# Optimization experiments

Measured on AMD Instinct MI355X. Metric: run time of the kernel, lower is better.

## Reference

```python
import jax, jax.numpy as jnp
import numpy as np

N = 65536   # num rois (batch*num_rois)
C = 512     # input_channels
D = 512     # output_dims = num_heads * head_dims
H = 8       # num_heads
HD = 64     # head_dims
L = 16      # hardcoded expand size in forward
BN_EPS = 1e-5


def _bn(x, gamma, beta, mean, var):
    # eval-mode BatchNorm1d over channel axis 1 of [N, D, L]
    inv = gamma / jnp.sqrt(var + BN_EPS)
    return x * inv[None, :, None] + (beta - mean * inv)[None, :, None]


def setup_inputs() -> dict:
    key = jax.random.key(0)
    ks = jax.random.split(key, 12)
    w = lambda k, shape: jax.random.normal(k, shape, jnp.float32) * 0.05
    return {
        "features": jax.random.normal(ks[0], (N, C), jnp.float32),
        "features2": jax.random.normal(ks[1], (N, C), jnp.float32),
        "Wk": w(ks[2], (D, C)),      # key_proj conv1d weight (shared for pos & key)
        "Wv1": w(ks[3], (D, C)),     # value_proj conv1d #1
        "Wv2": w(ks[4], (D, D)),     # value_proj conv1d #2
        "bn1_gamma": jnp.ones((D,), jnp.float32),
        "bn1_beta": jnp.zeros((D,), jnp.float32),
        "bn1_mean": jax.random.normal(ks[5], (D,), jnp.float32) * 0.1,
        "bn1_var": jax.random.uniform(ks[6], (D,), jnp.float32, 0.5, 1.5),
        "bn2_gamma": jnp.ones((D,), jnp.float32),
        "bn2_beta": jnp.zeros((D,), jnp.float32),
        "bn2_mean": jax.random.normal(ks[7], (D,), jnp.float32) * 0.1,
        "bn2_var": jax.random.uniform(ks[8], (D,), jnp.float32, 0.5, 1.5),
        "Wa": w(ks[9], (H, D)),      # attention_proj conv1d
        "Wqk": w(ks[10], (D, D)),    # qk_coef Linear
        "Wvc": w(ks[11], (D, D)),    # v_coef Linear
    }


def reference(features, features2, Wk, Wv1, Wv2,
              bn1_gamma, bn1_beta, bn1_mean, bn1_var,
              bn2_gamma, bn2_beta, bn2_mean, bn2_var,
              Wa, Wqk, Wvc):
    # expand [N, C] -> [N, C, L] (all L columns identical, as in torch .expand)
    f = jnp.broadcast_to(features[:, :, None], (features.shape[0], features.shape[1], L))
    f2 = jnp.broadcast_to(features2[:, :, None], (features2.shape[0], features2.shape[1], L))

    # key_proj (shared weights) on both inputs: 1x1 conv + ReLU
    pos = jax.nn.relu(jnp.einsum('oc,ncl->nol', Wk, f))
    key_e = jax.nn.relu(jnp.einsum('oc,ncl->nol', Wk, f2))

    # value_proj: conv -> BN -> ReLU -> conv -> BN -> ReLU
    h = jax.nn.relu(_bn(jnp.einsum('oc,ncl->nol', Wv1, f2), bn1_gamma, bn1_beta, bn1_mean, bn1_var))
    value = jax.nn.relu(_bn(jnp.einsum('od,ndl->nol', Wv2, h), bn2_gamma, bn2_beta, bn2_mean, bn2_var))

    pk = pos * key_e                                    # [N, D, L]
    v_coef = jax.nn.sigmoid(pos.mean(axis=2) @ Wvc.T)   # [N, D]
    qk_coef = jax.nn.sigmoid(pk.mean(axis=2) @ Wqk.T)   # [N, D]

    value = value + pos * v_coef[:, :, None]
    attn_emb = pk * qk_coef[:, :, None]

    attn = jnp.einsum('hd,ndl->nhl', Wa, attn_emb)      # [N, H, L]
    attn = jax.nn.softmax(attn, axis=-1)
    attn = jnp.repeat(attn, HD, axis=1)                 # [N, H*HD, L], head-major

    return jnp.sum(attn * value, axis=-1)               # [N, D]
```

## Files before the change

### kernel.cpp

```cpp
#include <hip/hip_runtime.h>
#include <hip/hip_bf16.h>
#include <cstdint>
#include <cstddef>


#define DIM 512
#define NROWS 65536
#define MBLK 64

typedef __bf16 bf16;
typedef __attribute__((ext_vector_type(8))) __bf16 bf16x8;
typedef __attribute__((ext_vector_type(4))) __bf16 bf16x4;
typedef __attribute__((ext_vector_type(4))) float f32x4;

__device__ __forceinline__ float sigmoidf_(float x) {
  return 1.0f / (1.0f + __expf(-x));
}

__device__ __forceinline__ int lds_off(int row, int cb) {
  return row * (DIM * 2) + (cb ^ ((row & 15) << 4));
}

__device__ __forceinline__ bf16x8 lda(const char* As, int i, int lr, int kq,
                                      int kb) {
  return *(const bf16x8*)(As + (i * 16 + lr) * (DIM * 2) +
                          ((kb * 2 + kq * 16) ^ (lr << 4)));
}

__global__ __launch_bounds__(256) void cvt4_f32_bf16(
    const float* __restrict__ s0, const float* __restrict__ s1,
    const float* __restrict__ s2, const float* __restrict__ s3,
    bf16* __restrict__ d0, bf16* __restrict__ d1, bf16* __restrict__ d2,
    bf16* __restrict__ d3) {
  int mat = blockIdx.x >> 8;
  int i = (blockIdx.x & 255) * 256 + threadIdx.x;
  const float* s = mat == 0 ? s0 : mat == 1 ? s1 : mat == 2 ? s2 : s3;
  bf16* d = mat == 0 ? d0 : mat == 1 ? d1 : mat == 2 ? d2 : d3;
  f32x4 v = ((const f32x4*)s)[i];
  bf16x4 o;
  o[0] = (bf16)v[0]; o[1] = (bf16)v[1]; o[2] = (bf16)v[2]; o[3] = (bf16)v[3];
  ((bf16x4*)d)[i] = o;
}

__device__ __forceinline__ void stage2(char* PA, const float* __restrict__ ga,
                                       char* PB, const float* __restrict__ gb,
                                       int t) {
#pragma unroll
  for (int it = 0; it < 4; ++it) {
    int c = it * 1024 + t;
    f32x4 a0 = *(const f32x4*)(ga + (size_t)c * 8);
    f32x4 a1 = *(const f32x4*)(ga + (size_t)c * 8 + 4);
    f32x4 b0 = *(const f32x4*)(gb + (size_t)c * 8);
    f32x4 b1 = *(const f32x4*)(gb + (size_t)c * 8 + 4);
    bf16x8 oa, ob;
    oa[0] = (bf16)a0[0]; oa[1] = (bf16)a0[1]; oa[2] = (bf16)a0[2]; oa[3] = (bf16)a0[3];
    oa[4] = (bf16)a1[0]; oa[5] = (bf16)a1[1]; oa[6] = (bf16)a1[2]; oa[7] = (bf16)a1[3];
    ob[0] = (bf16)b0[0]; ob[1] = (bf16)b0[1]; ob[2] = (bf16)b0[2]; ob[3] = (bf16)b0[3];
    ob[4] = (bf16)b1[0]; ob[5] = (bf16)b1[1]; ob[6] = (bf16)b1[2]; ob[7] = (bf16)b1[3];
    int off = lds_off(c >> 6, (c & 63) * 16);
    *(bf16x8*)(PA + off) = oa;
    *(bf16x8*)(PB + off) = ob;
  }
}

__device__ __forceinline__ void gemm_core(f32x4 (&acc)[4][2], const char* As,
                                          const bf16* __restrict__ W, int lr,
                                          int kq, int wn) {
  const bf16* bp = W + (size_t)(wn + lr) * DIM + kq * 8;
  bf16x8 a0[4], a1[4], b0[2], b1[2];
#pragma unroll
  for (int j = 0; j < 2; j++) b0[j] = *(const bf16x8*)(bp + j * 16 * DIM);
#pragma unroll
  for (int j = 0; j < 2; j++) b1[j] = *(const bf16x8*)(bp + j * 16 * DIM + 32);
#pragma unroll
  for (int i = 0; i < 4; i++) a0[i] = lda(As, i, lr, kq, 0);
#pragma unroll
  for (int kb = 0; kb < DIM; kb += 64) {
#pragma unroll
    for (int i = 0; i < 4; i++) a1[i] = lda(As, i, lr, kq, kb + 32);
#pragma unroll
    for (int i = 0; i < 4; i++)
#pragma unroll
      for (int j = 0; j < 2; j++)
        acc[i][j] = __builtin_amdgcn_mfma_f32_16x16x32_bf16(a0[i], b0[j],
                                                            acc[i][j], 0, 0, 0);
    if (kb + 64 < DIM) {
#pragma unroll
      for (int j = 0; j < 2; j++)
        b0[j] = *(const bf16x8*)(bp + j * 16 * DIM + kb + 64);
#pragma unroll
      for (int i = 0; i < 4; i++) a0[i] = lda(As, i, lr, kq, kb + 64);
    }
#pragma unroll
    for (int i = 0; i < 4; i++)
#pragma unroll
      for (int j = 0; j < 2; j++)
        acc[i][j] = __builtin_amdgcn_mfma_f32_16x16x32_bf16(a1[i], b1[j],
                                                            acc[i][j], 0, 0, 0);
    if (kb + 96 < DIM) {
#pragma unroll
      for (int j = 0; j < 2; j++)
        b1[j] = *(const bf16x8*)(bp + j * 16 * DIM + kb + 96);
    }
  }
}

__device__ __forceinline__ void zero_acc(f32x4 (&acc)[4][2]) {
#pragma unroll
  for (int i = 0; i < 4; i++)
#pragma unroll
    for (int j = 0; j < 2; j++) acc[i][j] = (f32x4){0.f, 0.f, 0.f, 0.f};
}

__global__ __launch_bounds__(1024, 1) void fused_all(
    const float* __restrict__ f, const float* __restrict__ f2,
    const bf16* __restrict__ Wk, const bf16* __restrict__ Wvc,
    const bf16* __restrict__ Wv1, const bf16* __restrict__ Wv2,
    float* __restrict__ out, const float* __restrict__ bg1,
    const float* __restrict__ bb1, const float* __restrict__ bm1,
    const float* __restrict__ bv1, const float* __restrict__ bg2,
    const float* __restrict__ bb2, const float* __restrict__ bm2,
    const float* __restrict__ bv2) {
  __shared__ __align__(16) char P1[MBLK * DIM * 2];
  __shared__ __align__(16) char P2[MBLK * DIM * 2];

  const int t = threadIdx.x;
  const int lane = t & 63;
  const int lr = lane & 15;
  const int kq = lane >> 4;
  const int wn = (t >> 6) * 32;
  const size_t m0 = (size_t)blockIdx.x * MBLK;

  stage2(P1, f + m0 * DIM, P2, f2 + m0 * DIM, t);
  __syncthreads();

  f32x4 acc[4][2];

  zero_acc(acc);
  gemm_core(acc, P1, Wk, lr, kq, wn);
  __syncthreads();
#pragma unroll
  for (int i = 0; i < 4; i++)
#pragma unroll
    for (int j = 0; j < 2; j++)
#pragma unroll
      for (int r = 0; r < 4; r++) {
        int m = i * 16 + kq * 4 + r;
        int n = wn + j * 16 + lr;
        *(bf16*)(P1 + lds_off(m, n * 2)) = (bf16)fmaxf(acc[i][j][r], 0.f);
      }
  __syncthreads();

  zero_acc(acc);
  gemm_core(acc, P1, Wvc, lr, kq, wn);
  bf16x4 pvr[4][2];
#pragma unroll
  for (int i = 0; i < 4; i++)
#pragma unroll
    for (int j = 0; j < 2; j++)
#pragma unroll
      for (int r = 0; r < 4; r++) {
        int m = i * 16 + kq * 4 + r;
        int n = wn + j * 16 + lr;
        float p = (float)(*(const bf16*)(P1 + lds_off(m, n * 2)));
        pvr[i][j][r] = (bf16)(sigmoidf_(acc[i][j][r]) * p);
      }

  zero_acc(acc);
  gemm_core(acc, P2, Wv1, lr, kq, wn);
  float iv1[2], bc1[2];
#pragma unroll
  for (int j = 0; j < 2; j++) {
    int c = wn + j * 16 + lr;
    float s = bg1[c] * rsqrtf(bv1[c] + 1e-5f);
    iv1[j] = s;
    bc1[j] = bb1[c] - bm1[c] * s;
  }
  __syncthreads();
#pragma unroll
  for (int i = 0; i < 4; i++)
#pragma unroll
    for (int j = 0; j < 2; j++)
#pragma unroll
      for (int r = 0; r < 4; r++) {
        int m = i * 16 + kq * 4 + r;
        int n = wn + j * 16 + lr;
        float v = fmaxf(acc[i][j][r] * iv1[j] + bc1[j], 0.f);
        *(bf16*)(P2 + lds_off(m, n * 2)) = (bf16)v;
      }
  __syncthreads();

  zero_acc(acc);
  gemm_core(acc, P2, Wv2, lr, kq, wn);
  float iv2[2], bc2[2];
#pragma unroll
  for (int j = 0; j < 2; j++) {
    int c = wn + j * 16 + lr;
    float s = bg2[c] * rsqrtf(bv2[c] + 1e-5f);
    iv2[j] = s;
    bc2[j] = bb2[c] - bm2[c] * s;
  }
#pragma unroll
  for (int i = 0; i < 4; i++)
#pragma unroll
    for (int j = 0; j < 2; j++)
#pragma unroll
      for (int r = 0; r < 4; r++) {
        int m = i * 16 + kq * 4 + r;
        int n = wn + j * 16 + lr;
        float v = fmaxf(acc[i][j][r] * iv2[j] + bc2[j], 0.f) + (float)pvr[i][j][r];
        out[(m0 + m) * DIM + n] = v;
      }
}

extern "C" void kernel_launch(void* const* d_in, const int* in_sizes, int n_in,
                              void* d_out, int out_size, void* d_ws,
                              size_t ws_size, hipStream_t stream) {
  const float* features  = (const float*)d_in[0];
  const float* features2 = (const float*)d_in[1];
  const float* Wk  = (const float*)d_in[2];
  const float* Wv1 = (const float*)d_in[3];
  const float* Wv2 = (const float*)d_in[4];
  const float* g1 = (const float*)d_in[5];
  const float* b1 = (const float*)d_in[6];
  const float* m1 = (const float*)d_in[7];
  const float* v1 = (const float*)d_in[8];
  const float* g2 = (const float*)d_in[9];
  const float* b2 = (const float*)d_in[10];
  const float* m2 = (const float*)d_in[11];
  const float* v2 = (const float*)d_in[12];
  const float* Wvc = (const float*)d_in[15];
  float* out = (float*)d_out;

  bf16* wkb  = (bf16*)d_ws;
  bf16* wvcb = wkb + (size_t)DIM * DIM;
  bf16* wv1b = wvcb + (size_t)DIM * DIM;
  bf16* wv2b = wv1b + (size_t)DIM * DIM;

  cvt4_f32_bf16<<<dim3(4 * 256), dim3(256), 0, stream>>>(
      Wk, Wvc, Wv1, Wv2, wkb, wvcb, wv1b, wv2b);

  dim3 grid(NROWS / MBLK);
  dim3 block(1024);
  fused_all<<<grid, block, 0, stream>>>(features, features2, wkb, wvcb, wv1b,
                                        wv2b, out, g1, b1, m1, v1, g2, b2, m2,
                                        v2);
}
```

Measured before the change: 664.5 us.

## Split fused kernel into two kernels with pv intermediate in workspace

Splits the single fused kernel into two. The first computes the pos and v_coef path and writes the gated pos*v_coef product to a bf16 workspace. The second computes the value path and adds the stored product. This halves LDS per block from 128KB to 64KB and removes the live pvr registers across GEMMs, which could allow two blocks per CU despite launch_bounds(1024,1). The cost is an extra round trip of a 64MB intermediate through global memory and a second launch.

```diff
diff --git a/kernel.cpp b/kernel.cpp
--- a/kernel.cpp
+++ b/kernel.cpp
@@ -42,24 +42,17 @@
   ((bf16x4*)d)[i] = o;
 }
 
-__device__ __forceinline__ void stage2(char* PA, const float* __restrict__ ga,
-                                       char* PB, const float* __restrict__ gb,
-                                       int t) {
+__device__ __forceinline__ void stage_panel(char* P, const float* __restrict__ g,
+                                            int t) {
 #pragma unroll
   for (int it = 0; it < 4; ++it) {
     int c = it * 1024 + t;
-    f32x4 a0 = *(const f32x4*)(ga + (size_t)c * 8);
-    f32x4 a1 = *(const f32x4*)(ga + (size_t)c * 8 + 4);
-    f32x4 b0 = *(const f32x4*)(gb + (size_t)c * 8);
-    f32x4 b1 = *(const f32x4*)(gb + (size_t)c * 8 + 4);
-    bf16x8 oa, ob;
-    oa[0] = (bf16)a0[0]; oa[1] = (bf16)a0[1]; oa[2] = (bf16)a0[2]; oa[3] = (bf16)a0[3];
-    oa[4] = (bf16)a1[0]; oa[5] = (bf16)a1[1]; oa[6] = (bf16)a1[2]; oa[7] = (bf16)a1[3];
-    ob[0] = (bf16)b0[0]; ob[1] = (bf16)b0[1]; ob[2] = (bf16)b0[2]; ob[3] = (bf16)b0[3];
-    ob[4] = (bf16)b1[0]; ob[5] = (bf16)b1[1]; ob[6] = (bf16)b1[2]; ob[7] = (bf16)b1[3];
-    int off = lds_off(c >> 6, (c & 63) * 16);
-    *(bf16x8*)(PA + off) = oa;
-    *(bf16x8*)(PB + off) = ob;
+    f32x4 v0 = *(const f32x4*)(g + (size_t)c * 8);
+    f32x4 v1 = *(const f32x4*)(g + (size_t)c * 8 + 4);
+    bf16x8 o;
+    o[0] = (bf16)v0[0]; o[1] = (bf16)v0[1]; o[2] = (bf16)v0[2]; o[3] = (bf16)v0[3];
+    o[4] = (bf16)v1[0]; o[5] = (bf16)v1[1]; o[6] = (bf16)v1[2]; o[7] = (bf16)v1[3];
+    *(bf16x8*)(P + lds_off(c >> 6, (c & 63) * 16)) = o;
   }
 }
 
@@ -112,17 +105,10 @@
     for (int j = 0; j < 2; j++) acc[i][j] = (f32x4){0.f, 0.f, 0.f, 0.f};
 }
 
-__global__ __launch_bounds__(1024, 1) void fused_all(
-    const float* __restrict__ f, const float* __restrict__ f2,
-    const bf16* __restrict__ Wk, const bf16* __restrict__ Wvc,
-    const bf16* __restrict__ Wv1, const bf16* __restrict__ Wv2,
-    float* __restrict__ out, const float* __restrict__ bg1,
-    const float* __restrict__ bb1, const float* __restrict__ bm1,
-    const float* __restrict__ bv1, const float* __restrict__ bg2,
-    const float* __restrict__ bb2, const float* __restrict__ bm2,
-    const float* __restrict__ bv2) {
-  __shared__ __align__(16) char P1[MBLK * DIM * 2];
-  __shared__ __align__(16) char P2[MBLK * DIM * 2];
+__global__ __launch_bounds__(1024, 1) void fusedA(
+    const float* __restrict__ f, const bf16* __restrict__ Wk,
+    const bf16* __restrict__ Wvc, bf16x4* __restrict__ pvws) {
+  __shared__ __align__(16) char P[MBLK * DIM * 2];
 
   const int t = threadIdx.x;
   const int lane = t & 63;
@@ -131,13 +117,13 @@
   const int wn = (t >> 6) * 32;
   const size_t m0 = (size_t)blockIdx.x * MBLK;
 
-  stage2(P1, f + m0 * DIM, P2, f2 + m0 * DIM, t);
+  stage_panel(P, f + m0 * DIM, t);
   __syncthreads();
 
   f32x4 acc[4][2];
 
   zero_acc(acc);
-  gemm_core(acc, P1, Wk, lr, kq, wn);
+  gemm_core(acc, P, Wk, lr, kq, wn);
   __syncthreads();
 #pragma unroll
   for (int i = 0; i < 4; i++)
@@ -147,27 +133,52 @@
       for (int r = 0; r < 4; r++) {
         int m = i * 16 + kq * 4 + r;
         int n = wn + j * 16 + lr;
-        *(bf16*)(P1 + lds_off(m, n * 2)) = (bf16)fmaxf(acc[i][j][r], 0.f);
-      }
-  __syncthreads();
-
-  zero_acc(acc);
-  gemm_core(acc, P1, Wvc, lr, kq, wn);
-  bf16x4 pvr[4][2];
-#pragma unroll
-  for (int i = 0; i < 4; i++)
-#pragma unroll
-    for (int j = 0; j < 2; j++)
-#pragma unroll
-      for (int r = 0; r < 4; r++) {
-        int m = i * 16 + kq * 4 + r;
-        int n = wn + j * 16 + lr;
-        float p = (float)(*(const bf16*)(P1 + lds_off(m, n * 2)));
-        pvr[i][j][r] = (bf16)(sigmoidf_(acc[i][j][r]) * p);
-      }
-
-  zero_acc(acc);
-  gemm_core(acc, P2, Wv1, lr, kq, wn);
+        *(bf16*)(P + lds_off(m, n * 2)) = (bf16)fmaxf(acc[i][j][r], 0.f);
+      }
+  __syncthreads();
+
+  zero_acc(acc);
+  gemm_core(acc, P, Wvc, lr, kq, wn);
+#pragma unroll
+  for (int i = 0; i < 4; i++)
+#pragma unroll
+    for (int j = 0; j < 2; j++) {
+      bf16x4 o;
+#pragma unroll
+      for (int r = 0; r < 4; r++) {
+        int m = i * 16 + kq * 4 + r;
+        int n = wn + j * 16 + lr;
+        float p = (float)(*(const bf16*)(P + lds_off(m, n * 2)));
+        o[r] = (bf16)(sigmoidf_(acc[i][j][r]) * p);
+      }
+      pvws[((size_t)blockIdx.x * 8 + i * 2 + j) * 1024 + t] = o;
+    }
+}
+
+__global__ __launch_bounds__(1024, 1) void fusedB(
+    const float* __restrict__ f2, const bf16* __restrict__ Wv1,
+    const bf16* __restrict__ Wv2, const bf16x4* __restrict__ pvws,
+    float* __restrict__ out, const float* __restrict__ bg1,
+    const float* __restrict__ bb1, const float* __restrict__ bm1,
+    const float* __restrict__ bv1, const float* __restrict__ bg2,
+    const float* __restrict__ bb2, const float* __restrict__ bm2,
+    const float* __restrict__ bv2) {
+  __shared__ __align__(16) char P[MBLK * DIM * 2];
+
+  const int t = threadIdx.x;
+  const int lane = t & 63;
+  const int lr = lane & 15;
+  const int kq = lane >> 4;
+  const int wn = (t >> 6) * 32;
+  const size_t m0 = (size_t)blockIdx.x * MBLK;
+
+  stage_panel(P, f2 + m0 * DIM, t);
+  __syncthreads();
+
+  f32x4 acc[4][2];
+
+  zero_acc(acc);
+  gemm_core(acc, P, Wv1, lr, kq, wn);
   float iv1[2], bc1[2];
 #pragma unroll
   for (int j = 0; j < 2; j++) {
@@ -186,12 +197,12 @@
         int m = i * 16 + kq * 4 + r;
         int n = wn + j * 16 + lr;
         float v = fmaxf(acc[i][j][r] * iv1[j] + bc1[j], 0.f);
-        *(bf16*)(P2 + lds_off(m, n * 2)) = (bf16)v;
-      }
-  __syncthreads();
-
-  zero_acc(acc);
-  gemm_core(acc, P2, Wv2, lr, kq, wn);
+        *(bf16*)(P + lds_off(m, n * 2)) = (bf16)v;
+      }
+  __syncthreads();
+
+  zero_acc(acc);
+  gemm_core(acc, P, Wv2, lr, kq, wn);
   float iv2[2], bc2[2];
 #pragma unroll
   for (int j = 0; j < 2; j++) {
@@ -203,14 +214,16 @@
 #pragma unroll
   for (int i = 0; i < 4; i++)
 #pragma unroll
-    for (int j = 0; j < 2; j++)
-#pragma unroll
-      for (int r = 0; r < 4; r++) {
-        int m = i * 16 + kq * 4 + r;
-        int n = wn + j * 16 + lr;
-        float v = fmaxf(acc[i][j][r] * iv2[j] + bc2[j], 0.f) + (float)pvr[i][j][r];
+    for (int j = 0; j < 2; j++) {
+      bf16x4 pv = pvws[((size_t)blockIdx.x * 8 + i * 2 + j) * 1024 + t];
+#pragma unroll
+      for (int r = 0; r < 4; r++) {
+        int m = i * 16 + kq * 4 + r;
+        int n = wn + j * 16 + lr;
+        float v = fmaxf(acc[i][j][r] * iv2[j] + bc2[j], 0.f) + (float)pv[r];
         out[(m0 + m) * DIM + n] = v;
       }
+    }
 }
 
 extern "C" void kernel_launch(void* const* d_in, const int* in_sizes, int n_in,
@@ -236,13 +249,15 @@
   bf16* wvcb = wkb + (size_t)DIM * DIM;
   bf16* wv1b = wvcb + (size_t)DIM * DIM;
   bf16* wv2b = wv1b + (size_t)DIM * DIM;
+  bf16* pvws = wv2b + (size_t)DIM * DIM;
 
   cvt4_f32_bf16<<<dim3(4 * 256), dim3(256), 0, stream>>>(
       Wk, Wvc, Wv1, Wv2, wkb, wvcb, wv1b, wv2b);
 
   dim3 grid(NROWS / MBLK);
   dim3 block(1024);
-  fused_all<<<grid, block, 0, stream>>>(features, features2, wkb, wvcb, wv1b,
-                                        wv2b, out, g1, b1, m1, v1, g2, b2, m2,
-                                        v2);
-}
+  fusedA<<<grid, block, 0, stream>>>(features, wkb, wvcb, (bf16x4*)pvws);
+  fusedB<<<grid, block, 0, stream>>>(features2, wv1b, wv2b,
+                                     (const bf16x4*)pvws, out,
+                                     g1, b1, m1, v1, g2, b2, m2, v2);
+}
```

New measurement: 608.5 us. -8.4%, faster.
